# Kernel optimization log

Hardware: AMD Instinct MI355X
Metric: run time of the kernel (lower is better)

## Reference

```python
import jax, jax.numpy as jnp
import numpy as np

A = 5.0  # smoothness parameter from init_kwargs


def setup_inputs() -> dict:
    key = jax.random.key(0)
    k1, k2 = jax.random.split(key)
    x = jax.random.uniform(k1, (512, 512), dtype=jnp.float32)        # [B, in_features]
    weight = jax.random.uniform(k2, (512, 1024), dtype=jnp.float32)  # [in_features, out_features]
    return {"x": x, "weight": weight}


def reference(x, weight):
    # inner[b, i, o] = max(x[b, i], weight[i, o])
    inner = jnp.maximum(x[..., :, None], weight[None])  # [B, I, O]
    # hard min over in_features
    hard = jnp.min(inner, axis=-2)                       # [B, O]
    # smooth (log-sum-exp) soft-min over in_features
    smooth = -jax.nn.logsumexp(-A * inner, axis=-2) / A  # [B, O]
    # STE: forward value == hard, gradient flows through smooth
    return hard - jax.lax.stop_gradient(smooth) + smooth
```

## Files before the change

### kernel.cpp

```cpp
#include <hip/hip_runtime.h>


#define B_DIM 512
#define I_DIM 512
#define O_DIM 1024
#define NBUCK 256
#define U 8

#define LOADC(K, XS, W)                                                            \
  _Pragma("unroll") for (int u = 0; u < U; ++u) {                                  \
    const unsigned long long kk = s[(K) + u];   \
    const int row = __builtin_amdgcn_readfirstlane((int)(unsigned)kk);             \
    const unsigned xb = (unsigned)__builtin_amdgcn_readfirstlane((int)(kk >> 32)); \
    XS[u] = __uint_as_float(xb);                                                   \
    W[u] = w[(size_t)row * O_DIM + o];          \
  }

__global__ __launch_bounds__(1024, 8) void SmoothSTEMinMax_fused(
    const float* __restrict__ x,
    const float* __restrict__ w,
    float* __restrict__ out) {
  __shared__ unsigned int hist[NBUCK];
  __shared__ unsigned int wssum[4];
  __shared__ unsigned long long s[I_DIM];

  const int t = threadIdx.x;
  const int b = blockIdx.x;
  const int lane = t & 63;

  float xval = 0.0f;
  int bb = 0;
  if (t < I_DIM) {
    xval = x[b * I_DIM + t];
    bb = (int)(xval * 256.0f);
    bb = bb > 255 ? 255 : (bb < 0 ? 0 : bb);
  }
  if (t < NBUCK) hist[t] = 0;
  __syncthreads();
  if (t < I_DIM) atomicAdd(&hist[bb], 1u);
  __syncthreads();

  unsigned v = 0, cnt = 0;
  if (t < NBUCK) {
    cnt = hist[t];
    v = cnt;
#pragma unroll
    for (int d = 1; d < 64; d <<= 1) {
      const unsigned n = __shfl_up(v, d, 64);
      if (lane >= d) v += n;
    }
    if (lane == 63) wssum[t >> 6] = v;
  }
  __syncthreads();
  if (t < NBUCK) {
    unsigned add = 0;
#pragma unroll
    for (int ww = 0; ww < 4; ++ww)
      if (ww < (t >> 6)) add += wssum[ww];
    hist[t] = v + add - cnt;
  }
  __syncthreads();
  if (t < I_DIM) {
    const unsigned pos = atomicAdd(&hist[bb], 1u);
    s[pos] = ((unsigned long long)__float_as_uint(xval) << 32) | (unsigned)t;
  }
  __syncthreads();

  const int o = t;
  float A = 3.402823466e+38f;

  float xsA[U], xsB[U];
  float wA[U], wB[U];

  LOADC(0, xsA, wA);
  int k = 0;
  while (true) {
    {
      const bool last = (k + U >= I_DIM);
      if (!last) LOADC(k + U, xsB, wB);
#pragma unroll
      for (int u = 0; u < U; ++u) A = fminf(A, fmaxf(xsA[u], wA[u]));
      k += U;
      if (last) break;
      const int bn = (int)(xsB[0] * 256.0f);
      const float thresh = (float)bn * 0.00390625f;
      if (!__any(A > thresh)) break;
    }
    {
      const bool last = (k + U >= I_DIM);
      if (!last) LOADC(k + U, xsA, wA);
#pragma unroll
      for (int u = 0; u < U; ++u) A = fminf(A, fmaxf(xsB[u], wB[u]));
      k += U;
      if (last) break;
      const int bn = (int)(xsA[0] * 256.0f);
      const float thresh = (float)bn * 0.00390625f;
      if (!__any(A > thresh)) break;
    }
  }

  out[b * O_DIM + o] = A;
}

extern "C" void kernel_launch(void* const* d_in, const int* in_sizes, int n_in,
                              void* d_out, int out_size, void* d_ws, size_t ws_size,
                              hipStream_t stream) {
  const float* x = (const float*)d_in[0];
  const float* w = (const float*)d_in[1];
  float* out = (float*)d_out;

  SmoothSTEMinMax_fused<<<B_DIM, 1024, 0, stream>>>(x, w, out);
}
```

Baseline: 14.21 us.

## Preload first 128 sorted entries into lane registers and read via readlane

Stores the sorted x entries as a precomputed byte offset plus x value. Each lane loads a uint4 from LDS once, covering the first 128 entries, and broadcasts them with v_readlane instead of per-entry LDS reads plus readfirstlane. The first 64 entries are processed without early-exit checks and the next 64 with checks every 8. A fallback loop reads LDS for the remainder. The aim is lower LDS traffic and less address arithmetic in the early-exit hot loop, at the cost of always doing 64 entries and dropping the double-buffered weight prefetch.

```diff
diff --git a/kernel.cpp b/kernel.cpp
--- a/kernel.cpp
+++ b/kernel.cpp
@@ -5,16 +5,8 @@
 #define I_DIM 512
 #define O_DIM 1024
 #define NBUCK 256
-#define U 8
 
-#define LOADC(K, XS, W)                                                            \
-  _Pragma("unroll") for (int u = 0; u < U; ++u) {                                  \
-    const unsigned long long kk = s[(K) + u];   \
-    const int row = __builtin_amdgcn_readfirstlane((int)(unsigned)kk);             \
-    const unsigned xb = (unsigned)__builtin_amdgcn_readfirstlane((int)(kk >> 32)); \
-    XS[u] = __uint_as_float(xb);                                                   \
-    W[u] = w[(size_t)row * O_DIM + o];          \
-  }
+#define RL(v_, l_) ((unsigned)__builtin_amdgcn_readlane((int)(v_), (l_)))
 
 __global__ __launch_bounds__(1024, 8) void SmoothSTEMinMax_fused(
     const float* __restrict__ x,
@@ -22,7 +14,7 @@
     float* __restrict__ out) {
   __shared__ unsigned int hist[NBUCK];
   __shared__ unsigned int wssum[4];
-  __shared__ unsigned long long s[I_DIM];
+  __shared__ unsigned int sdat[2 * I_DIM];
 
   const int t = threadIdx.x;
   const int b = blockIdx.x;
@@ -62,44 +54,69 @@
   __syncthreads();
   if (t < I_DIM) {
     const unsigned pos = atomicAdd(&hist[bb], 1u);
-    s[pos] = ((unsigned long long)__float_as_uint(xval) << 32) | (unsigned)t;
+    sdat[2 * pos] = (unsigned)t * (unsigned)(O_DIM * 4);
+    sdat[2 * pos + 1] = __float_as_uint(xval);
   }
   __syncthreads();
 
-  const int o = t;
+  const unsigned o4 = (unsigned)t * 4u;
+  const char* wb = reinterpret_cast<const char*>(w);
   float A = 3.402823466e+38f;
 
-  float xsA[U], xsB[U];
-  float wA[U], wB[U];
+  const uint4 q = *reinterpret_cast<const uint4*>(&sdat[4 * lane]);
 
-  LOADC(0, xsA, wA);
-  int k = 0;
-  while (true) {
-    {
-      const bool last = (k + U >= I_DIM);
-      if (!last) LOADC(k + U, xsB, wB);
 #pragma unroll
-      for (int u = 0; u < U; ++u) A = fminf(A, fmaxf(xsA[u], wA[u]));
-      k += U;
-      if (last) break;
-      const int bn = (int)(xsB[0] * 256.0f);
-      const float thresh = (float)bn * 0.00390625f;
-      if (!__any(A > thresh)) break;
+  for (int c = 0; c < 8; ++c) {
+    float wv[8], xv[8];
+#pragma unroll
+    for (int e = 0; e < 8; ++e) {
+      const int g = c * 8 + e;
+      const unsigned off = RL((g & 1) ? q.z : q.x, g >> 1);
+      const unsigned xb  = RL((g & 1) ? q.w : q.y, g >> 1);
+      xv[e] = __uint_as_float(xb);
+      wv[e] = *reinterpret_cast<const float*>(wb + (off + o4));
     }
-    {
-      const bool last = (k + U >= I_DIM);
-      if (!last) LOADC(k + U, xsA, wA);
 #pragma unroll
-      for (int u = 0; u < U; ++u) A = fminf(A, fmaxf(xsB[u], wB[u]));
-      k += U;
-      if (last) break;
-      const int bn = (int)(xsA[0] * 256.0f);
-      const float thresh = (float)bn * 0.00390625f;
-      if (!__any(A > thresh)) break;
+    for (int e = 0; e < 8; ++e) A = fminf(A, fmaxf(xv[e], wv[e]));
+  }
+
+  int k = 64;
+#pragma unroll
+  for (int c = 8; c < 16; ++c) {
+    const float nx = __uint_as_float(RL(q.y, 4 * c));
+    const float th = (float)(int)(nx * 256.0f) * 0.00390625f;
+    if (!__any(A > th)) break;
+#pragma unroll
+    for (int e = 0; e < 8; ++e) {
+      const int g = c * 8 + e;
+      const unsigned off = RL((g & 1) ? q.z : q.x, g >> 1);
+      const unsigned xb  = RL((g & 1) ? q.w : q.y, g >> 1);
+      const float wvv = *reinterpret_cast<const float*>(wb + (off + o4));
+      A = fminf(A, fmaxf(__uint_as_float(xb), wvv));
+    }
+    k += 8;
+  }
+
+  if (k >= 128) {
+    while (k < I_DIM) {
+      const float nx = __uint_as_float(
+          (unsigned)__builtin_amdgcn_readfirstlane((int)sdat[2 * k + 1]));
+      const float th = (float)(int)(nx * 256.0f) * 0.00390625f;
+      if (!__any(A > th)) break;
+#pragma unroll
+      for (int u = 0; u < 8; ++u) {
+        const unsigned off =
+            (unsigned)__builtin_amdgcn_readfirstlane((int)sdat[2 * (k + u)]);
+        const unsigned xb =
+            (unsigned)__builtin_amdgcn_readfirstlane((int)sdat[2 * (k + u) + 1]);
+        const float wvv = *reinterpret_cast<const float*>(wb + (off + o4));
+        A = fminf(A, fmaxf(__uint_as_float(xb), wvv));
+      }
+      k += 8;
     }
   }
 
-  out[b * O_DIM + o] = A;
+  out[b * O_DIM + t] = A;
 }
 
 extern "C" void kernel_launch(void* const* d_in, const int* in_sizes, int n_in,
```

Result: faster. 13.62 us (-4.1%).
